# Kernel optimization log

Hardware: AMD Instinct MI355X
Metric: run time of the kernel (lower is better)

The kernel has to match this reference:

```python
import jax, jax.numpy as jnp
import numpy as np
from jax import lax

B, S, MAX_WORD = 64, 40, 25
L = S * MAX_WORD            # 1000 tokens
D_IN, D = 768, 256
G = 6                       # lda_group_num
KW, KS = 5, 3               # word / sentence conv kernel sizes


def _conv1d(x, W, b, pad):
    # x: (B, Cin, L), W: (Cout, Cin, K) -> (B, Cout, L) ('same' via explicit pad)
    y = lax.conv_general_dilated(x, W, window_strides=(1,), padding=[(pad, pad)],
                                 dimension_numbers=('NCH', 'OIH', 'NCH'))
    return y + b[None, :, None]


def _mha(x, Wq, bq, Wk, bk, Wv, bv, Wo, bo):
    # single-head self-attention; x: (batch, seq, D)
    q = x @ Wq + bq
    k = x @ Wk + bk
    v = x @ Wv + bv
    scores = jnp.einsum('bqd,bkd->bqk', q, k) / jnp.sqrt(jnp.asarray(D, x.dtype))
    attn = jax.nn.softmax(scores, axis=-1)
    out = jnp.einsum('bqk,bkd->bqd', attn, v)
    return out @ Wo + bo


def setup_inputs() -> dict:
    key = jax.random.key(0)
    ks = jax.random.split(key, 32)
    s = 0.05
    p = lambda k, shape: jax.random.normal(k, shape, jnp.float32) * s
    x = jax.random.normal(ks[0], (B, D_IN, L), jnp.float32)
    lda = jax.random.randint(ks[1], (B, S), 0, G)
    # guarantee each group non-empty per row (original would NaN on empty groups)
    lda = lda.at[:, :G].set(jnp.broadcast_to(jnp.arange(G), (B, G)))
    inp = {'x': x, 'lda_groups': lda,
           'Wc_w': p(ks[2], (D, D_IN, KW)), 'bc_w': p(ks[3], (D,)),
           'Wq_w': p(ks[4], (D, D)), 'bq_w': p(ks[5], (D,)),
           'Wk_w': p(ks[6], (D, D)), 'bk_w': p(ks[7], (D,)),
           'Wv_w': p(ks[8], (D, D)), 'bv_w': p(ks[9], (D,)),
           'Wo_w': p(ks[10], (D, D)), 'bo_w': p(ks[11], (D,)),
           'Wc_s': p(ks[12], (D, D, KS)), 'bc_s': p(ks[13], (D,)),
           'Wq_s': p(ks[14], (D, D)), 'bq_s': p(ks[15], (D,)),
           'Wk_s': p(ks[16], (D, D)), 'bk_s': p(ks[17], (D,)),
           'Wv_s': p(ks[18], (D, D)), 'bv_s': p(ks[19], (D,)),
           'Wo_s': p(ks[20], (D, D)), 'bo_s': p(ks[21], (D,)),
           'Wq_a': p(ks[22], (D, D)), 'bq_a': p(ks[23], (D,)),
           'Wk_a': p(ks[24], (D, D)), 'bk_a': p(ks[25], (D,)),
           'Wv_a': p(ks[26], (D, D)), 'bv_a': p(ks[27], (D,)),
           'Wo_a': p(ks[28], (D, D)), 'bo_a': p(ks[29], (D,))}
    return inp


def reference(x, lda_groups, Wc_w, bc_w, Wq_w, bq_w, Wk_w, bk_w, Wv_w, bv_w, Wo_w, bo_w,
              Wc_s, bc_s, Wq_s, bq_s, Wk_s, bk_s, Wv_s, bv_s, Wo_s, bo_s,
              Wq_a, bq_a, Wk_a, bk_a, Wv_a, bv_a, Wo_a, bo_a):
    # word-level CNN (dropout = identity in eval) + attention gate
    h = jax.nn.relu(_conv1d(x, Wc_w, bc_w, (KW - 1) // 2))      # (B, D, L)
    h = jnp.transpose(h, (0, 2, 1))                              # (B, L, D)
    h = h * _mha(h, Wq_w, bq_w, Wk_w, bk_w, Wv_w, bv_w, Wo_w, bo_w)
    # word_level_mean: contiguous blocks of MAX_WORD words -> sentence vectors
    h = h.reshape(B, S, MAX_WORD, D).mean(axis=2)                # (B, S, D)
    # sentence-level CNN
    h = jnp.transpose(h, (0, 2, 1))
    h = jax.nn.relu(_conv1d(h, Wc_s, bc_s, (KS - 1) // 2))
    h = jnp.transpose(h, (0, 2, 1))                              # (B, S, D)
    # sentence attention: torch MHA has batch_first=False but gets (B,S,D),
    # i.e. it attends over the batch axis with S as batch -> transpose
    ht = jnp.transpose(h, (1, 0, 2))
    a = jnp.transpose(_mha(ht, Wq_s, bq_s, Wk_s, bk_s, Wv_s, bv_s, Wo_s, bo_s), (1, 0, 2))
    h = h * a
    # aspect_level_mean (faithful to the original bug): per (batch, group) the
    # mean is a SCALAR over selected sentences AND all channels, broadcast to D
    mask = (lda_groups[:, :, None] == jnp.arange(G)[None, None, :]).astype(h.dtype)  # (B,S,G)
    gsum = jnp.einsum('bs,bsg->bg', h.sum(-1), mask)
    cnt = mask.sum(axis=1) * D
    ha = jnp.broadcast_to((gsum / cnt)[:, :, None], (B, G, D))   # (B, G, D)
    # aspect attention applied twice with the SAME params; same batch_first quirk
    for _ in range(2):
        hat = jnp.transpose(ha, (1, 0, 2))
        a = jnp.transpose(_mha(hat, Wq_a, bq_a, Wk_a, bk_a, Wv_a, bv_a, Wo_a, bo_a), (1, 0, 2))
        ha = ha * a
    return ha
```

## Files before the change

### kernel.cpp

```cpp
#include <hip/hip_runtime.h>
#include <hip/hip_bf16.h>


typedef unsigned short u16;
typedef __attribute__((ext_vector_type(8))) short bf16x8;
typedef __attribute__((ext_vector_type(4))) float f32x4;
typedef __attribute__((ext_vector_type(4))) unsigned short u16x4;
typedef __attribute__((ext_vector_type(8))) unsigned short u16x8;

__device__ __forceinline__ float bf2f(u16 u) {
  union { float f; unsigned int i; } x; x.i = ((unsigned int)u) << 16; return x.f;
}
__device__ __forceinline__ u16 f2bf(float f) {
  union { float f; unsigned int i; } x; x.f = f;
  unsigned int i = x.i;
  i += 0x7FFFu + ((i >> 16) & 1u);
  return (u16)(i >> 16);
}
__device__ __forceinline__ void gload16(const u16* g, u16* l) {
  __builtin_amdgcn_global_load_lds(
      (const __attribute__((address_space(1))) unsigned int*)g,
      (__attribute__((address_space(3))) unsigned int*)l, 16, 0, 0);
}

__global__ __launch_bounds__(256) void prep_weights_kernel(
    const float* __restrict__ Wc_w, const float* __restrict__ Wq_w,
    const float* __restrict__ Wk_w, const float* __restrict__ Wv_w,
    const float* __restrict__ Wo_w, const float* __restrict__ bq_w,
    const float* __restrict__ bk_w, const float* __restrict__ bv_w,
    const float* __restrict__ Wc_s,
    u16* __restrict__ WtT, u16* __restrict__ WqkvT, u16* __restrict__ WoT,
    float* __restrict__ bqkv, float* __restrict__ Wts)
{
  int idx = blockIdx.x * 256 + threadIdx.x;
  if (idx < 983040) {
    int n = idx / 3840, kk = idx % 3840;
    int k = kk / 768, c = kk % 768;
    WtT[idx] = f2bf(Wc_w[n * 3840 + c * 5 + k]);
  }
  if (idx < 196608) {
    int n = idx >> 8, kd = idx & 255;
    float v = (n < 256) ? Wq_w[kd * 256 + n]
            : (n < 512) ? Wk_w[kd * 256 + (n - 256)]
                        : Wv_w[kd * 256 + (n - 512)];
    WqkvT[idx] = f2bf(v);
  }
  if (idx < 65536) {
    int n = idx >> 8, kd = idx & 255;
    WoT[idx] = f2bf(Wo_w[kd * 256 + n]);
  }
  if (idx < 768) {
    bqkv[idx] = (idx < 256) ? bq_w[idx] : (idx < 512) ? bk_w[idx - 256] : bv_w[idx - 512];
  }
  if (idx < 196608) {
    int kk = idx >> 8, d = idx & 255;
    int k = kk >> 8, dc = kk & 255;
    Wts[idx] = Wc_s[d * 768 + dc * 3 + k];
  }
}

__global__ __launch_bounds__(256) void zero_pad_kernel(u16* __restrict__ xT)
{
  int c8 = blockIdx.x * 256 + threadIdx.x;
  if (c8 >= 172032) return;
  int e = c8 * 8;
  int b = e / 21504, rem = e % 21504;
  int rowi = rem / 768, c = rem % 768;
  int row = (rowi < 2) ? rowi : (1000 + rowi);
  u16x8 z = {0, 0, 0, 0, 0, 0, 0, 0};
  *(u16x8*)&xT[((size_t)b * 1028 + row) * 768 + c] = z;
}

__global__ __launch_bounds__(256) void transpose_x_kernel(const float* __restrict__ x,
                                                          u16* __restrict__ xT)
{
  __shared__ float lds[64][65];
  int t = threadIdx.x;
  int bid = blockIdx.x;
  int b = bid / 192, rem = bid % 192;
  int c0 = (rem / 16) * 64, l0 = (rem % 16) * 64;
  int pr = t >> 4, plc = (t & 15) * 4;
  #pragma unroll
  for (int i = 0; i < 4; i++) {
    int r = i * 16 + pr;
    f32x4 v = {0.f, 0.f, 0.f, 0.f};
    if (l0 + plc < 1000)
      v = *(const f32x4*)&x[((size_t)b * 768 + c0 + r) * 1000 + l0 + plc];
    lds[r][plc + 0] = v[0]; lds[r][plc + 1] = v[1];
    lds[r][plc + 2] = v[2]; lds[r][plc + 3] = v[3];
  }
  __syncthreads();
  int qr = t >> 3, qc = (t & 7) * 8;
  #pragma unroll
  for (int i = 0; i < 2; i++) {
    int l = i * 32 + qr;
    if (l0 + l < 1000) {
      u16x8 o;
      #pragma unroll
      for (int j = 0; j < 8; j++) o[j] = f2bf(lds[qc + j][l]);
      *(u16x8*)&xT[((size_t)b * 1028 + 2 + l0 + l) * 768 + c0 + qc] = o;
    }
  }
}

__global__ __launch_bounds__(256) void transpose_v_kernel(const u16* __restrict__ qkv,
                                                          u16* __restrict__ vT)
{
  __shared__ u16 lds[64][65];
  int t = threadIdx.x;
  int b = blockIdx.x >> 6, rem = blockIdx.x & 63;
  int d0 = (rem >> 4) * 64, kv0 = (rem & 15) * 64;
  int pr = t >> 4, plc = (t & 15) * 4;
  #pragma unroll
  for (int i = 0; i < 4; i++) {
    int kvl = i * 16 + pr;
    int kv = kv0 + kvl;
    u16x4 v = {0, 0, 0, 0};
    if (kv < 1000)
      v = *(const u16x4*)&qkv[((size_t)(b * 1000) + kv) * 768 + 512 + d0 + plc];
    lds[kvl][plc + 0] = v[0]; lds[kvl][plc + 1] = v[1];
    lds[kvl][plc + 2] = v[2]; lds[kvl][plc + 3] = v[3];
  }
  __syncthreads();
  int qr = t >> 3, qc = (t & 7) * 8;
  #pragma unroll
  for (int i = 0; i < 2; i++) {
    int d = i * 32 + qr;
    u16x8 o;
    #pragma unroll
    for (int j = 0; j < 8; j++) o[j] = lds[qc + j][d];
    *(u16x8*)&vT[((size_t)(b * 256) + d0 + d) * 1024 + kv0 + qc] = o;
  }
}

__global__ __launch_bounds__(512, 4) void conv_tap_kernel(
    const u16* __restrict__ A, const u16* __restrict__ Bt,
    const float* __restrict__ bias, u16* __restrict__ C)
{
  __shared__ u16 strip[144 * 64];
  __shared__ u16 Blds[256 * 64];
  int t = threadIdx.x;
  int wave = t >> 6, lane = t & 63;
  int l15 = lane & 15, l4 = lane >> 4;
  int mt = blockIdx.x;
  int wm = (wave >> 2) * 64, wn = (wave & 3) * 64;

  int nA = (wave < 2) ? 3 : 2;
  unsigned int aoff[3]; int aldsoff[3];
  #pragma unroll
  for (int i = 0; i < 3; i++) {
    int rc = wave + i * 8;
    if (rc > 17) rc = 17;
    int lr = rc * 8 + (lane >> 3);
    int ss = (lane & 7) ^ (lr & 7);
    int gm = mt * 128 + lr;
    aoff[i] = (unsigned int)((gm >> 10) * 789504 + (gm & 1023) * 768 + ss * 8);
    aldsoff[i] = rc * 512;
  }
  unsigned int boff[4]; int bldsoff[4];
  #pragma unroll
  for (int i = 0; i < 4; i++) {
    int c = wave * 4 + i;
    int lr = c * 8 + (lane >> 3);
    int ss = (lane & 7) ^ (lr & 7);
    boff[i] = (unsigned int)(lr * 3840 + ss * 8);
    bldsoff[i] = c * 512;
  }

  f32x4 acc[4][4];
  #pragma unroll
  for (int mf = 0; mf < 4; mf++)
    #pragma unroll
    for (int nf = 0; nf < 4; nf++) acc[mf][nf] = f32x4{0.f, 0.f, 0.f, 0.f};

  for (int ch = 0; ch < 12; ch++) {
    unsigned int co = (unsigned int)(ch * 64);
    #pragma unroll
    for (int i = 0; i < 3; i++)
      if (i < nA) gload16(A + aoff[i] + co, &strip[aldsoff[i]]);
    #pragma unroll 1
    for (int tap = 0; tap < 5; tap++) {
      unsigned int bo = (unsigned int)(tap * 768) + co;
      #pragma unroll
      for (int i = 0; i < 4; i++) gload16(Bt + boff[i] + bo, &Blds[bldsoff[i]]);
      __syncthreads();
      #pragma unroll
      for (int kc = 0; kc < 2; kc++) {
        int q = kc * 4 + l4;
        bf16x8 af[4], bfr[4];
        #pragma unroll
        for (int mf = 0; mf < 4; mf++) {
          int rr = wm + mf * 16 + l15 + tap;
          af[mf] = *(const bf16x8*)(&strip[rr * 64 + ((q ^ (rr & 7)) * 8)]);
        }
        #pragma unroll
        for (int nf = 0; nf < 4; nf++) {
          int rb = wn + nf * 16 + l15;
          bfr[nf] = *(const bf16x8*)(&Blds[rb * 64 + ((q ^ (rb & 7)) * 8)]);
        }
        #pragma unroll
        for (int mf = 0; mf < 4; mf++)
          #pragma unroll
          for (int nf = 0; nf < 4; nf++)
            acc[mf][nf] = __builtin_amdgcn_mfma_f32_16x16x32_bf16(af[mf], bfr[nf], acc[mf][nf], 0, 0, 0);
      }
      __syncthreads();
    }
  }

  float bv[4];
  #pragma unroll
  for (int nf = 0; nf < 4; nf++) bv[nf] = bias[wn + nf * 16 + l15];
  #pragma unroll
  for (int mf = 0; mf < 4; mf++) {
    #pragma unroll
    for (int r = 0; r < 4; r++) {
      int rowl = wm + mf * 16 + l4 * 4 + r;
      int gm = mt * 128 + rowl;
      int bb = gm >> 10, ll = gm & 1023;
      if (ll < 1000) {
        size_t orow = (size_t)bb * 1000 + ll;
        #pragma unroll
        for (int nf = 0; nf < 4; nf++) {
          float v = fmaxf(acc[mf][nf][r] + bv[nf], 0.f);
          C[orow * 256 + wn + nf * 16 + l15] = f2bf(v);
        }
      }
    }
  }
}

template<bool RELU>
__global__ __launch_bounds__(512, 4) void gemm_bf16_kernel(
    const u16* __restrict__ A, const u16* __restrict__ Bt,
    const float* __restrict__ bias, u16* __restrict__ C,
    int lda, int K, int nk, int ntiles, int ldc)
{
  __shared__ u16 Alds[128 * 64];
  __shared__ u16 Blds[256 * 64];
  int t = threadIdx.x;
  int wave = t >> 6, lane = t & 63;
  int l15 = lane & 15, l4 = lane >> 4;
  int mt = blockIdx.x / ntiles, nt = blockIdx.x % ntiles;
  int wm = (wave >> 2) * 64, wn = (wave & 3) * 64;

  unsigned int aoff[2]; int aldsoff[2];
  #pragma unroll
  for (int i = 0; i < 2; i++) {
    int c = wave * 2 + i;
    int lr = c * 8 + (lane >> 3);
    int ss = (lane & 7) ^ (lr & 7);
    int gm = mt * 128 + lr;
    aoff[i] = (unsigned int)gm * (unsigned int)lda + (unsigned int)(ss * 8);
    aldsoff[i] = c * 512;
  }
  unsigned int boff[4]; int bldsoff[4];
  #pragma unroll
  for (int i = 0; i < 4; i++) {
    int c = wave * 4 + i;
    int lr = c * 8 + (lane >> 3);
    int ss = (lane & 7) ^ (lr & 7);
    boff[i] = (unsigned int)(nt * 256 + lr) * (unsigned int)K + (unsigned int)(ss * 8);
    bldsoff[i] = c * 512;
  }

  f32x4 acc[4][4];
  #pragma unroll
  for (int mf = 0; mf < 4; mf++)
    #pragma unroll
    for (int nf = 0; nf < 4; nf++) acc[mf][nf] = f32x4{0.f, 0.f, 0.f, 0.f};

  for (int ks = 0; ks < nk; ks++) {
    unsigned int ko = (unsigned int)ks * 64u;
    #pragma unroll
    for (int i = 0; i < 2; i++) gload16(A + aoff[i] + ko, &Alds[aldsoff[i]]);
    #pragma unroll
    for (int i = 0; i < 4; i++) gload16(Bt + boff[i] + ko, &Blds[bldsoff[i]]);
    __syncthreads();
    #pragma unroll
    for (int kc = 0; kc < 2; kc++) {
      int q = kc * 4 + l4;
      bf16x8 af[4], bfr[4];
      #pragma unroll
      for (int mf = 0; mf < 4; mf++) {
        int r = wm + mf * 16 + l15;
        af[mf] = *(const bf16x8*)(&Alds[r * 64 + ((q ^ (r & 7)) * 8)]);
      }
      #pragma unroll
      for (int nf = 0; nf < 4; nf++) {
        int rb = wn + nf * 16 + l15;
        bfr[nf] = *(const bf16x8*)(&Blds[rb * 64 + ((q ^ (rb & 7)) * 8)]);
      }
      #pragma unroll
      for (int mf = 0; mf < 4; mf++)
        #pragma unroll
        for (int nf = 0; nf < 4; nf++)
          acc[mf][nf] = __builtin_amdgcn_mfma_f32_16x16x32_bf16(af[mf], bfr[nf], acc[mf][nf], 0, 0, 0);
    }
    __syncthreads();
  }
  float bv[4];
  #pragma unroll
  for (int nf = 0; nf < 4; nf++) bv[nf] = bias[nt * 256 + wn + nf * 16 + l15];
  #pragma unroll
  for (int mf = 0; mf < 4; mf++) {
    #pragma unroll
    for (int r = 0; r < 4; r++) {
      int rowl = wm + mf * 16 + l4 * 4 + r;
      size_t orow = (size_t)(mt * 128 + rowl);
      #pragma unroll
      for (int nf = 0; nf < 4; nf++) {
        float v = acc[mf][nf][r] + bv[nf];
        if (RELU) v = fmaxf(v, 0.f);
        C[orow * ldc + nt * 256 + wn + nf * 16 + l15] = f2bf(v);
      }
    }
  }
}

__global__ __launch_bounds__(256, 3) void flash_kernel(
    const u16* __restrict__ qkv, const u16* __restrict__ vT, u16* __restrict__ ctx)
{
  __shared__ u16 Klds[32 * 256];
  __shared__ u16 Vlds[256 * 32];
  __shared__ u16 Plds[4 * 640];
  int t = threadIdx.x, wave = t >> 6, lane = t & 63;
  int l15 = lane & 15, l4 = lane >> 4;
  int b = blockIdx.x >> 4, qt = blockIdx.x & 15;

  int qrow = qt * 64 + wave * 16 + l15;
  const u16* qp = qkv + ((size_t)(b * 1000) + qrow) * 768;
  bf16x8 qreg[8];
  #pragma unroll
  for (int kk = 0; kk < 8; kk++) qreg[kk] = *(const bf16x8*)(qp + kk * 32 + l4 * 8);

  f32x4 acc[16];
  #pragma unroll
  for (int df = 0; df < 16; df++) acc[df] = f32x4{0.f, 0.f, 0.f, 0.f};
  float tsum[4] = {0.f, 0.f, 0.f, 0.f};

  const u16* ksrc[4]; int kdst[4];
  const u16* vsrc[4]; int vdst[4];
  #pragma unroll
  for (int i = 0; i < 4; i++) {
    int c = i * 256 + t;
    int kr = c >> 5, kslot = c & 31;
    ksrc[i] = qkv + ((size_t)(b * 1000 + kr)) * 768 + 256 + kslot * 8;
    kdst[i] = kr * 256 + ((kslot ^ (kr & 7)) * 8);
    int vd = c >> 2, vslot = c & 3;
    vsrc[i] = vT + ((size_t)(b * 256 + vd)) * 1024 + vslot * 8;
    vdst[i] = vd * 32 + ((vslot ^ (vd & 3)) * 8);
  }
  bf16x8 kreg[4], vreg[4];
  #pragma unroll
  for (int i = 0; i < 4; i++) { kreg[i] = *(const bf16x8*)ksrc[i]; vreg[i] = *(const bf16x8*)vsrc[i]; }

  u16* pl = &Plds[wave * 640];

  for (int tile = 0; tile < 32; tile++) {
    __syncthreads();
    #pragma unroll
    for (int i = 0; i < 4; i++) {
      *(bf16x8*)(&Klds[kdst[i]]) = kreg[i];
      *(bf16x8*)(&Vlds[vdst[i]]) = vreg[i];
    }
    __syncthreads();
    if (tile + 1 < 32) {
      #pragma unroll
      for (int i = 0; i < 4; i++) {
        kreg[i] = *(const bf16x8*)(ksrc[i] + (size_t)(tile + 1) * 32 * 768);
        vreg[i] = *(const bf16x8*)(vsrc[i] + (tile + 1) * 32);
      }
    }
    f32x4 s[2];
    #pragma unroll
    for (int cf = 0; cf < 2; cf++) {
      s[cf] = f32x4{0.f, 0.f, 0.f, 0.f};
      int kr = cf * 16 + l15;
      #pragma unroll
      for (int kk = 0; kk < 8; kk++) {
        bf16x8 kf = *(const bf16x8*)(&Klds[kr * 256 + (((kk * 4 + l4) ^ (kr & 7)) * 8)]);
        s[cf] = __builtin_amdgcn_mfma_f32_16x16x32_bf16(qreg[kk], kf, s[cf], 0, 0, 0);
      }
    }
    int colb = tile * 32;
    float pv[2][4];
    #pragma unroll
    for (int r = 0; r < 4; r++) {
      float s0 = s[0][r] * 0.0625f;
      float s1 = s[1][r] * 0.0625f;
      if (colb + l15 >= 1000)      s0 = -1e30f;
      if (colb + 16 + l15 >= 1000) s1 = -1e30f;
      float p0 = __expf(s0 - 20.f);
      float p1 = __expf(s1 - 20.f);
      tsum[r] += p0 + p1;
      pv[0][r] = p0; pv[1][r] = p1;
    }
    #pragma unroll
    for (int cf = 0; cf < 2; cf++)
      #pragma unroll
      for (int r = 0; r < 4; r++)
        pl[(l4 * 4 + r) * 40 + cf * 16 + l15] = f2bf(pv[cf][r]);
    bf16x8 pa = *(const bf16x8*)(&pl[l15 * 40 + l4 * 8]);
    #pragma unroll
    for (int df = 0; df < 16; df++) {
      int d = df * 16 + l15;
      bf16x8 vf = *(const bf16x8*)(&Vlds[d * 32 + ((l4 ^ (d & 3)) * 8)]);
      acc[df] = __builtin_amdgcn_mfma_f32_16x16x32_bf16(pa, vf, acc[df], 0, 0, 0);
    }
  }
  #pragma unroll
  for (int r = 0; r < 4; r++) {
    float ts = tsum[r];
    #pragma unroll
    for (int mk = 1; mk < 16; mk <<= 1) ts += __shfl_xor(ts, mk, 16);
    tsum[r] = ts;
  }
  int orow0 = qt * 64 + wave * 16 + l4 * 4;
  #pragma unroll
  for (int r = 0; r < 4; r++) {
    int orow = orow0 + r;
    if (orow < 1000) {
      float inv = 1.0f / tsum[r];
      size_t base = ((size_t)(b * 1000) + orow) * 256;
      #pragma unroll
      for (int df = 0; df < 16; df++)
        ctx[base + df * 16 + l15] = f2bf(acc[df][r] * inv);
    }
  }
}

__global__ __launch_bounds__(256) void gate_mean_kernel(const u16* __restrict__ h,
                                                        const u16* __restrict__ ao,
                                                        u16* __restrict__ hmpad)
{
  int r = blockIdx.x, t = threadIdx.x;
  int b = r / 40, s = r % 40;
  size_t base = ((size_t)b * 1000 + s * 25) * 256 + t;
  float acc = 0.f;
  #pragma unroll 5
  for (int w = 0; w < 25; w++) acc += bf2f(h[base + (size_t)w * 256]) * bf2f(ao[base + (size_t)w * 256]);
  hmpad[((size_t)b * 42 + 1 + s) * 256 + t] = f2bf(acc * 0.04f);
}

__global__ __launch_bounds__(256) void sent_conv_kernel(const u16* __restrict__ hmpad,
                                                        const float* __restrict__ Wts,
                                                        const float* __restrict__ bc_s,
                                                        float* __restrict__ hs)
{
  __shared__ float alds[10 * 256];
  int t = threadIdx.x;
  int b = blockIdx.x / 5, s0 = (blockIdx.x % 5) * 8;
  #pragma unroll
  for (int i = 0; i < 10; i++)
    alds[i * 256 + t] = bf2f(hmpad[((size_t)b * 42 + s0 + i) * 256 + t]);
  __syncthreads();
  float acc[8]; float bv = bc_s[t];
  #pragma unroll
  for (int j = 0; j < 8; j++) acc[j] = bv;
  for (int kk = 0; kk < 768; kk++) {
    float w = Wts[(size_t)kk * 256 + t];
    #pragma unroll
    for (int j = 0; j < 8; j++) acc[j] += alds[j * 256 + kk] * w;
  }
  #pragma unroll
  for (int j = 0; j < 8; j++)
    hs[((size_t)b * 40 + s0 + j) * 256 + t] = fmaxf(acc[j], 0.f);
}

__global__ __launch_bounds__(256) void proj3_kernel(
    const float* __restrict__ A,
    const float* __restrict__ Wq, const float* __restrict__ bq,
    const float* __restrict__ Wk, const float* __restrict__ bk,
    const float* __restrict__ Wv, const float* __restrict__ bv,
    float* __restrict__ oq, float* __restrict__ okk, float* __restrict__ ov,
    int nb, int GS)
{
  __shared__ float alds[8 * 256];
  int sel = blockIdx.x / nb;
  int m0 = (blockIdx.x % nb) * 8;
  const float* W = (sel == 0) ? Wq : (sel == 1) ? Wk : Wv;
  const float* bias_ = (sel == 0) ? bq : (sel == 1) ? bk : bv;
  float* out = (sel == 0) ? oq : (sel == 1) ? okk : ov;
  int t = threadIdx.x;
  #pragma unroll
  for (int i = 0; i < 8; i++) {
    int r = m0 + i;
    int src = (r & 63) * GS + (r >> 6);
    alds[i * 256 + t] = A[(size_t)src * 256 + t];
  }
  __syncthreads();
  float acc[8]; float bv_ = bias_[t];
  #pragma unroll
  for (int i = 0; i < 8; i++) acc[i] = bv_;
  for (int k = 0; k < 256; k++) {
    float w = W[(size_t)k * 256 + t];
    #pragma unroll
    for (int i = 0; i < 8; i++) acc[i] += alds[i * 256 + k] * w;
  }
  #pragma unroll
  for (int i = 0; i < 8; i++) out[((size_t)m0 + i) * 256 + t] = acc[i];
}

__global__ __launch_bounds__(256) void attn_fused_kernel(
    const float* __restrict__ q, const float* __restrict__ k,
    const float* __restrict__ v, const float* __restrict__ Wo,
    const float* __restrict__ bo, const float* __restrict__ gate_src,
    float* __restrict__ out, int GS)
{
  __shared__ float pbuf[4][64];
  __shared__ float pvals[64];
  __shared__ float obuf[256];
  int r = blockIdx.x;
  int bb = r >> 6, i = r & 63;
  int t = threadIdx.x, tj = t & 63, part = t >> 6;
  const float* qrow = q + (size_t)r * 256 + part * 64;
  const float* krow = k + ((size_t)(bb * 64) + tj) * 256 + part * 64;
  float pp = 0.f;
  #pragma unroll 16
  for (int kk = 0; kk < 64; kk++) pp += qrow[kk] * krow[kk];
  pbuf[part][tj] = pp;
  __syncthreads();
  if (t < 64) {
    float s = (pbuf[0][t] + pbuf[1][t] + pbuf[2][t] + pbuf[3][t]) * 0.0625f;
    float mx = s;
    #pragma unroll
    for (int mk = 1; mk < 64; mk <<= 1) mx = fmaxf(mx, __shfl_xor(mx, mk, 64));
    float p = __expf(s - mx);
    float sm = p;
    #pragma unroll
    for (int mk = 1; mk < 64; mk <<= 1) sm += __shfl_xor(sm, mk, 64);
    pvals[t] = p / sm;
  }
  __syncthreads();
  float acc = 0.f;
  const float* vb = v + (size_t)(bb * 64) * 256 + t;
  for (int j = 0; j < 64; j++) acc += pvals[j] * vb[(size_t)j * 256];
  obuf[t] = acc;
  __syncthreads();
  float o = bo[t];
  for (int kk = 0; kk < 256; kk++) o += obuf[kk] * Wo[(size_t)kk * 256 + t];
  size_t gi = (size_t)i * GS + bb;
  out[gi * 256 + t] = gate_src[gi * 256 + t] * o;
}

__global__ __launch_bounds__(256) void aspect_mean_kernel(const float* __restrict__ h2,
                                                          const int* __restrict__ ldaG,
                                                          float* __restrict__ ha0)
{
  __shared__ float partbuf[6][256];
  __shared__ int ldas[40];
  __shared__ float gval[6];
  int b = blockIdx.x, t = threadIdx.x;
  if (t < 40) ldas[t] = ldaG[b * 40 + t];
  __syncthreads();
  float part[6] = {0, 0, 0, 0, 0, 0};
  for (int idx = t; idx < 10240; idx += 256) {
    int s = idx >> 8, d = idx & 255;
    float v = h2[((size_t)b * 40 + s) * 256 + d];
    int g = ldas[s];
    #pragma unroll
    for (int gg = 0; gg < 6; gg++) if (g == gg) part[gg] += v;
  }
  #pragma unroll
  for (int g = 0; g < 6; g++) partbuf[g][t] = part[g];
  __syncthreads();
  if (t < 6) {
    float ssum = 0.f;
    for (int i = 0; i < 256; i++) ssum += partbuf[t][i];
    int cnt = 0;
    for (int s = 0; s < 40; s++) cnt += (ldas[s] == t) ? 1 : 0;
    gval[t] = ssum / ((float)cnt * 256.0f);
  }
  __syncthreads();
  #pragma unroll
  for (int g = 0; g < 6; g++) ha0[((size_t)b * 6 + g) * 256 + t] = gval[g];
}

extern "C" void kernel_launch(void* const* d_in, const int* in_sizes, int n_in,
                              void* d_out, int out_size, void* d_ws, size_t ws_size,
                              hipStream_t stream) {
  (void)in_sizes; (void)n_in; (void)out_size; (void)ws_size;
  const float* x    = (const float*)d_in[0];
  const int*   ldaG = (const int*)d_in[1];
  const float* Wc_w = (const float*)d_in[2];
  const float* bc_w = (const float*)d_in[3];
  const float* Wq_w = (const float*)d_in[4];
  const float* bq_w = (const float*)d_in[5];
  const float* Wk_w = (const float*)d_in[6];
  const float* bk_w = (const float*)d_in[7];
  const float* Wv_w = (const float*)d_in[8];
  const float* bv_w = (const float*)d_in[9];
  const float* Wo_w = (const float*)d_in[10];
  const float* bo_w = (const float*)d_in[11];
  const float* Wc_s = (const float*)d_in[12];
  const float* bc_s = (const float*)d_in[13];
  const float* Wq_s = (const float*)d_in[14];
  const float* bq_s = (const float*)d_in[15];
  const float* Wk_s = (const float*)d_in[16];
  const float* bk_s = (const float*)d_in[17];
  const float* Wv_s = (const float*)d_in[18];
  const float* bv_s = (const float*)d_in[19];
  const float* Wo_s = (const float*)d_in[20];
  const float* bo_s = (const float*)d_in[21];
  const float* Wq_a = (const float*)d_in[22];
  const float* bq_a = (const float*)d_in[23];
  const float* Wk_a = (const float*)d_in[24];
  const float* bk_a = (const float*)d_in[25];
  const float* Wv_a = (const float*)d_in[26];
  const float* bv_a = (const float*)d_in[27];
  const float* Wo_a = (const float*)d_in[28];
  const float* bo_a = (const float*)d_in[29];

  char* ws = (char*)d_ws;
  u16*  xT    = (u16*)(ws + 0);
  u16*  qkvb  = (u16*)(ws + 0);
  u16*  attno = (u16*)(ws + 0);
  u16*  WtT   = (u16*)(ws + 101056512ULL);
  u16*  WqkvT = (u16*)(ws + 103022592ULL);
  u16*  WoT   = (u16*)(ws + 103415808ULL);
  float* bqkv = (float*)(ws + 103546880ULL);
  float* Wts  = (float*)(ws + 103549952ULL);
  u16*  h     = (u16*)(ws + 104336384ULL);
  u16*  ctx   = (u16*)(ws + 137104384ULL);
  u16*  vT    = (u16*)(ws + 169872384ULL);
  u16*  hmpad = (u16*)(ws + 203426816ULL);
  float* hs   = (float*)(ws + 204803072ULL);
  float* sq   = (float*)(ws + 207424512ULL);
  float* sk   = (float*)(ws + 210045952ULL);
  float* sv   = (float*)(ws + 212667392ULL);
  float* h2   = (float*)(ws + 215288832ULL);
  float* ha0  = (float*)(ws + 217910272ULL);
  float* aq   = (float*)(ws + 218303488ULL);
  float* ak   = (float*)(ws + 218696704ULL);
  float* av   = (float*)(ws + 219089920ULL);
  float* ha1  = (float*)(ws + 219483136ULL);

  hipMemsetAsync(hmpad, 0, 1376256ULL, stream);
  zero_pad_kernel<<<672, 256, 0, stream>>>(xT);

  prep_weights_kernel<<<3840, 256, 0, stream>>>(Wc_w, Wq_w, Wk_w, Wv_w, Wo_w,
                                                bq_w, bk_w, bv_w, Wc_s,
                                                WtT, WqkvT, WoT, bqkv, Wts);
  transpose_x_kernel<<<12288, 256, 0, stream>>>(x, xT);
  conv_tap_kernel<<<512, 512, 0, stream>>>(xT, WtT, bc_w, h);
  gemm_bf16_kernel<false><<<1500, 512, 0, stream>>>(h, WqkvT, bqkv, qkvb, 256, 256, 4, 3, 768);
  transpose_v_kernel<<<4096, 256, 0, stream>>>(qkvb, vT);
  flash_kernel<<<1024, 256, 0, stream>>>(qkvb, vT, ctx);
  gemm_bf16_kernel<false><<<500, 512, 0, stream>>>(ctx, WoT, bo_w, attno, 256, 256, 4, 1, 256);
  gate_mean_kernel<<<2560, 256, 0, stream>>>(h, attno, hmpad);
  sent_conv_kernel<<<320, 256, 0, stream>>>(hmpad, Wts, bc_s, hs);
  proj3_kernel<<<960, 256, 0, stream>>>(hs, Wq_s, bq_s, Wk_s, bk_s, Wv_s, bv_s,
                                        sq, sk, sv, 320, 40);
  attn_fused_kernel<<<2560, 256, 0, stream>>>(sq, sk, sv, Wo_s, bo_s, hs, h2, 40);
  aspect_mean_kernel<<<64, 256, 0, stream>>>(h2, ldaG, ha0);

  const float* hacur = ha0;
  for (int it = 0; it < 2; it++) {
    proj3_kernel<<<144, 256, 0, stream>>>(hacur, Wq_a, bq_a, Wk_a, bk_a, Wv_a, bv_a,
                                          aq, ak, av, 48, 6);
    float* dst = (it == 0) ? ha1 : (float*)d_out;
    attn_fused_kernel<<<384, 256, 0, stream>>>(aq, ak, av, Wo_a, bo_a, hacur, dst, 6);
    hacur = dst;
  }
}
```

Baseline: 636.1 us.

## Process two query fragments per wave in flash attention to double K/V reuse

Each wave in the flash kernel now computes 32 query rows (two 16-row MFMA fragments) against each staged K/V tile instead of 16, so each block covers 128 query rows and the grid halves from 1024 to 512 blocks. This halves global and LDS traffic for K and V per query row and issues two independent MFMAs per LDS fragment read. Block indices are remapped so consecutive blocks map to different batches. The cost is roughly double accumulator and Q register usage, with launch bounds lowered from 3 to 2 waves per SIMD, and fewer blocks in flight.

New measurement: 663.1 us. 4.2% more time.

```diff
diff --git a/kernel.cpp b/kernel.cpp
--- a/kernel.cpp
+++ b/kernel.cpp
@@ -318,114 +318,120 @@
   }
 }
 
-__global__ __launch_bounds__(256, 3) void flash_kernel(
+__global__ __launch_bounds__(256, 2) void flash_kernel(
     const u16* __restrict__ qkv, const u16* __restrict__ vT, u16* __restrict__ ctx)
 {
   __shared__ u16 Klds[32 * 256];
   __shared__ u16 Vlds[256 * 32];
-  __shared__ u16 Plds[4 * 640];
+  __shared__ u16 Plds[4 * 2 * 640];
   int t = threadIdx.x, wave = t >> 6, lane = t & 63;
   int l15 = lane & 15, l4 = lane >> 4;
-  int b = blockIdx.x >> 4, qt = blockIdx.x & 15;
-
-  int qrow = qt * 64 + wave * 16 + l15;
-  const u16* qp = qkv + ((size_t)(b * 1000) + qrow) * 768;
-  bf16x8 qreg[8];
-  #pragma unroll
-  for (int kk = 0; kk < 8; kk++) qreg[kk] = *(const bf16x8*)(qp + kk * 32 + l4 * 8);
-
-  f32x4 acc[16];
-  #pragma unroll
-  for (int df = 0; df < 16; df++) acc[df] = f32x4{0.f, 0.f, 0.f, 0.f};
-  float tsum[4] = {0.f, 0.f, 0.f, 0.f};
-
-  const u16* ksrc[4]; int kdst[4];
-  const u16* vsrc[4]; int vdst[4];
+  int old = blockIdx.x;
+  int b  = (old & 7) * 8 + ((old >> 3) & 7);
+  int qt = old >> 6;
+  size_t qbase = (size_t)b * 1000;
+
+  bf16x8 qreg[2][8];
+  #pragma unroll
+  for (int mf = 0; mf < 2; mf++) {
+    int qrow = qt * 128 + wave * 32 + mf * 16 + l15;
+    const u16* qp = qkv + (qbase + qrow) * 768;
+    #pragma unroll
+    for (int kk = 0; kk < 8; kk++)
+      qreg[mf][kk] = *(const bf16x8*)(qp + kk * 32 + l4 * 8);
+  }
+
+  f32x4 acc[2][16];
+  #pragma unroll
+  for (int mf = 0; mf < 2; mf++)
+    #pragma unroll
+    for (int df = 0; df < 16; df++) acc[mf][df] = f32x4{0.f, 0.f, 0.f, 0.f};
+  float tsum[2][4] = {{0.f,0.f,0.f,0.f},{0.f,0.f,0.f,0.f}};
+
+  bf16x8 kreg[4], vreg[4];
   #pragma unroll
   for (int i = 0; i < 4; i++) {
     int c = i * 256 + t;
     int kr = c >> 5, kslot = c & 31;
-    ksrc[i] = qkv + ((size_t)(b * 1000 + kr)) * 768 + 256 + kslot * 8;
-    kdst[i] = kr * 256 + ((kslot ^ (kr & 7)) * 8);
+    kreg[i] = *(const bf16x8*)(qkv + (qbase + kr) * 768 + 256 + kslot * 8);
     int vd = c >> 2, vslot = c & 3;
-    vsrc[i] = vT + ((size_t)(b * 256 + vd)) * 1024 + vslot * 8;
-    vdst[i] = vd * 32 + ((vslot ^ (vd & 3)) * 8);
-  }
-  bf16x8 kreg[4], vreg[4];
-  #pragma unroll
-  for (int i = 0; i < 4; i++) { kreg[i] = *(const bf16x8*)ksrc[i]; vreg[i] = *(const bf16x8*)vsrc[i]; }
-
-  u16* pl = &Plds[wave * 640];
+    vreg[i] = *(const bf16x8*)(vT + ((size_t)(b * 256) + vd) * 1024 + vslot * 8);
+  }
+
+  u16* pl0 = &Plds[wave * 1280];
+  u16* pl1 = pl0 + 640;
 
   for (int tile = 0; tile < 32; tile++) {
     __syncthreads();
     #pragma unroll
     for (int i = 0; i < 4; i++) {
-      *(bf16x8*)(&Klds[kdst[i]]) = kreg[i];
-      *(bf16x8*)(&Vlds[vdst[i]]) = vreg[i];
+      int c = i * 256 + t;
+      int kr = c >> 5, kslot = c & 31;
+      *(bf16x8*)(&Klds[kr * 256 + ((kslot ^ (kr & 7)) * 8)]) = kreg[i];
+      int vd = c >> 2, vslot = c & 3;
+      *(bf16x8*)(&Vlds[vd * 32 + ((vslot ^ (vd & 3)) * 8)]) = vreg[i];
     }
     __syncthreads();
     if (tile + 1 < 32) {
       #pragma unroll
       for (int i = 0; i < 4; i++) {
-        kreg[i] = *(const bf16x8*)(ksrc[i] + (size_t)(tile + 1) * 32 * 768);
-        vreg[i] = *(const bf16x8*)(vsrc[i] + (tile + 1) * 32);
-      }
-    }
-    f32x4 s[2];
+        int c = i * 256 + t;
+        int kr = c >> 5, kslot = c & 31;
+        kreg[i] = *(const bf16x8*)(qkv + (qbase + (tile + 1) * 32 + kr) * 768 + 256 + kslot * 8);
+        int vd = c >> 2, vslot = c & 3;
+        vreg[i] = *(const bf16x8*)(vT + ((size_t)(b * 256) + vd) * 1024 + (tile + 1) * 32 + vslot * 8);
+      }
+    }
     #pragma unroll
     for (int cf = 0; cf < 2; cf++) {
-      s[cf] = f32x4{0.f, 0.f, 0.f, 0.f};
+      f32x4 s0 = {0.f,0.f,0.f,0.f}, s1 = {0.f,0.f,0.f,0.f};
       int kr = cf * 16 + l15;
       #pragma unroll
       for (int kk = 0; kk < 8; kk++) {
         bf16x8 kf = *(const bf16x8*)(&Klds[kr * 256 + (((kk * 4 + l4) ^ (kr & 7)) * 8)]);
-        s[cf] = __builtin_amdgcn_mfma_f32_16x16x32_bf16(qreg[kk], kf, s[cf], 0, 0, 0);
-      }
-    }
-    int colb = tile * 32;
-    float pv[2][4];
-    #pragma unroll
-    for (int r = 0; r < 4; r++) {
-      float s0 = s[0][r] * 0.0625f;
-      float s1 = s[1][r] * 0.0625f;
-      if (colb + l15 >= 1000)      s0 = -1e30f;
-      if (colb + 16 + l15 >= 1000) s1 = -1e30f;
-      float p0 = __expf(s0 - 20.f);
-      float p1 = __expf(s1 - 20.f);
-      tsum[r] += p0 + p1;
-      pv[0][r] = p0; pv[1][r] = p1;
-    }
-    #pragma unroll
-    for (int cf = 0; cf < 2; cf++)
-      #pragma unroll
-      for (int r = 0; r < 4; r++)
-        pl[(l4 * 4 + r) * 40 + cf * 16 + l15] = f2bf(pv[cf][r]);
-    bf16x8 pa = *(const bf16x8*)(&pl[l15 * 40 + l4 * 8]);
+        s0 = __builtin_amdgcn_mfma_f32_16x16x32_bf16(qreg[0][kk], kf, s0, 0, 0, 0);
+        s1 = __builtin_amdgcn_mfma_f32_16x16x32_bf16(qreg[1][kk], kf, s1, 0, 0, 0);
+      }
+      bool colok = (tile * 32 + cf * 16 + l15) < 1000;
+      #pragma unroll
+      for (int r = 0; r < 4; r++) {
+        float p0 = colok ? __expf(s0[r] * 0.0625f - 20.f) : 0.f;
+        float p1 = colok ? __expf(s1[r] * 0.0625f - 20.f) : 0.f;
+        tsum[0][r] += p0; tsum[1][r] += p1;
+        pl0[(l4 * 4 + r) * 40 + cf * 16 + l15] = f2bf(p0);
+        pl1[(l4 * 4 + r) * 40 + cf * 16 + l15] = f2bf(p1);
+      }
+    }
+    bf16x8 pa0 = *(const bf16x8*)(&pl0[l15 * 40 + l4 * 8]);
+    bf16x8 pa1 = *(const bf16x8*)(&pl1[l15 * 40 + l4 * 8]);
     #pragma unroll
     for (int df = 0; df < 16; df++) {
       int d = df * 16 + l15;
       bf16x8 vf = *(const bf16x8*)(&Vlds[d * 32 + ((l4 ^ (d & 3)) * 8)]);
-      acc[df] = __builtin_amdgcn_mfma_f32_16x16x32_bf16(pa, vf, acc[df], 0, 0, 0);
-    }
-  }
-  #pragma unroll
-  for (int r = 0; r < 4; r++) {
-    float ts = tsum[r];
-    #pragma unroll
-    for (int mk = 1; mk < 16; mk <<= 1) ts += __shfl_xor(ts, mk, 16);
-    tsum[r] = ts;
-  }
-  int orow0 = qt * 64 + wave * 16 + l4 * 4;
-  #pragma unroll
-  for (int r = 0; r < 4; r++) {
-    int orow = orow0 + r;
-    if (orow < 1000) {
-      float inv = 1.0f / tsum[r];
-      size_t base = ((size_t)(b * 1000) + orow) * 256;
-      #pragma unroll
-      for (int df = 0; df < 16; df++)
-        ctx[base + df * 16 + l15] = f2bf(acc[df][r] * inv);
+      acc[0][df] = __builtin_amdgcn_mfma_f32_16x16x32_bf16(pa0, vf, acc[0][df], 0, 0, 0);
+      acc[1][df] = __builtin_amdgcn_mfma_f32_16x16x32_bf16(pa1, vf, acc[1][df], 0, 0, 0);
+    }
+  }
+  #pragma unroll
+  for (int mf = 0; mf < 2; mf++) {
+    #pragma unroll
+    for (int r = 0; r < 4; r++) {
+      float ts = tsum[mf][r];
+      #pragma unroll
+      for (int mk = 1; mk < 16; mk <<= 1) ts += __shfl_xor(ts, mk, 16);
+      tsum[mf][r] = ts;
+    }
+    int orow0 = qt * 128 + wave * 32 + mf * 16 + l4 * 4;
+    #pragma unroll
+    for (int r = 0; r < 4; r++) {
+      int orow = orow0 + r;
+      if (orow < 1000) {
+        float inv = 1.0f / tsum[mf][r];
+        size_t base = (qbase + orow) * 256;
+        #pragma unroll
+        for (int df = 0; df < 16; df++)
+          ctx[base + df * 16 + l15] = f2bf(acc[mf][df][r] * inv);
+      }
     }
   }
 }
@@ -646,7 +652,7 @@
   conv_tap_kernel<<<512, 512, 0, stream>>>(xT, WtT, bc_w, h);
   gemm_bf16_kernel<false><<<1500, 512, 0, stream>>>(h, WqkvT, bqkv, qkvb, 256, 256, 4, 3, 768);
   transpose_v_kernel<<<4096, 256, 0, stream>>>(qkvb, vT);
-  flash_kernel<<<1024, 256, 0, stream>>>(qkvb, vT, ctx);
+  flash_kernel<<<512, 256, 0, stream>>>(qkvb, vT, ctx);
   gemm_bf16_kernel<false><<<500, 512, 0, stream>>>(ctx, WoT, bo_w, attno, 256, 256, 4, 1, 256);
   gate_mean_kernel<<<2560, 256, 0, stream>>>(h, attno, hmpad);
   sent_conv_kernel<<<320, 256, 0, stream>>>(hmpad, Wts, bc_s, hs);
```
